# Performance work log

Hardware: AMD Instinct MI355X
Metric: run time of the kernel (lower is better)

The kernel has to match this reference:

```python
import jax, jax.numpy as jnp
import numpy as np

B, T, FB, C = 2, 256, 128, 128
H_T, H_F, BAND = 4, 4, 16
INNER = 4 * C


def setup_inputs() -> dict:
    key = jax.random.key(0)
    ks = jax.random.split(key, 8)
    g = lambda k, shp: jax.random.normal(k, shp, jnp.float32) * 0.02
    return {
        "x": jax.random.normal(ks[0], (B, T, FB, C), jnp.float32),
        # temporal pre-norm + MHA (in_proj [3C,C], out_proj [C,C])
        "ln_t_w": jnp.ones((C,), jnp.float32), "ln_t_b": jnp.zeros((C,), jnp.float32),
        "t_wi": g(ks[1], (3 * C, C)), "t_bi": jnp.zeros((3 * C,), jnp.float32),
        "t_wo": g(ks[2], (C, C)), "t_bo": jnp.zeros((C,), jnp.float32),
        # frequency pre-norm + MHA
        "ln_f_w": jnp.ones((C,), jnp.float32), "ln_f_b": jnp.zeros((C,), jnp.float32),
        "f_wi": g(ks[3], (3 * C, C)), "f_bi": jnp.zeros((3 * C,), jnp.float32),
        "f_wo": g(ks[4], (C, C)), "f_bo": jnp.zeros((C,), jnp.float32),
        # FFN pre-norm + two linears
        "ln_n_w": jnp.ones((C,), jnp.float32), "ln_n_b": jnp.zeros((C,), jnp.float32),
        "w1": g(ks[5], (INNER, C)), "b1": jnp.zeros((INNER,), jnp.float32),
        "w2": g(ks[6], (C, INNER)), "b2": jnp.zeros((C,), jnp.float32),
    }


def _ln(x, w, b, eps=1e-5):
    mu = x.mean(-1, keepdims=True)
    var = ((x - mu) ** 2).mean(-1, keepdims=True)
    return (x - mu) * jax.lax.rsqrt(var + eps) * w + b


def _mha(x, wi, bi, wo, bo, h, mask):
    """torch.nn.MultiheadAttention equivalent. x: [..., S, C], mask: additive [S, S]."""
    c = x.shape[-1]
    dh = c // h
    qkv = x @ wi.T + bi
    q, k, v = jnp.split(qkv, 3, axis=-1)
    split = lambda t: t.reshape(t.shape[:-1] + (h, dh)).swapaxes(-2, -3)  # [..., h, S, dh]
    q, k, v = split(q), split(k), split(v)
    scores = jnp.einsum('...hqd,...hkd->...hqk', q, k) * (1.0 / np.sqrt(dh)) + mask
    attn = jax.nn.softmax(scores, axis=-1)
    o = jnp.einsum('...hqk,...hkd->...hqd', attn, v)
    o = o.swapaxes(-2, -3).reshape(x.shape)
    return o @ wo.T + bo


def _causal_mask(n):
    i = jnp.arange(n)
    return jnp.where(i[:, None] >= i[None, :], 0.0, -jnp.inf).astype(jnp.float32)


def _band_mask(n, band):
    i = jnp.arange(n)
    return jnp.where(jnp.abs(i[:, None] - i[None, :]) <= band, 0.0, -jnp.inf).astype(jnp.float32)


def reference(x, ln_t_w, ln_t_b, t_wi, t_bi, t_wo, t_bo,
              ln_f_w, ln_f_b, f_wi, f_bi, f_wo, f_bo,
              ln_n_w, ln_n_b, w1, b1, w2, b2):
    cm = _causal_mask(x.shape[1])      # [T, T]
    bm = _band_mask(x.shape[2], BAND)  # [F, F]
    # temporal causal MHSA per frequency bin (pre-norm residual)
    xt = _ln(x, ln_t_w, ln_t_b).transpose(0, 2, 1, 3)  # [B, F, T, C]
    x = x + _mha(xt, t_wi, t_bi, t_wo, t_bo, H_T, cm).transpose(0, 2, 1, 3)
    # banded local MHSA over frequency per time step
    xf = _ln(x, ln_f_w, ln_f_b)  # [B, T, F, C]
    x = x + _mha(xf, f_wi, f_bi, f_wo, f_bo, H_F, bm)
    # FFN (Linear -> exact GELU -> Linear)
    xn = _ln(x, ln_n_w, ln_n_b)
    h = jax.nn.gelu(xn @ w1.T + b1, approximate=False)
    x = x + (h @ w2.T + b2)
    return x
```

## Files before the change

kernel.cpp:

```cpp
#include <hip/hip_runtime.h>
#include <math.h>

typedef __bf16 bf16;
typedef __bf16 bf16x8 __attribute__((ext_vector_type(8)));
typedef __bf16 bf16x4 __attribute__((ext_vector_type(4)));
typedef __bf16 bf16x2 __attribute__((ext_vector_type(2)));
typedef float f32x4 __attribute__((ext_vector_type(4)));
typedef float f32x2 __attribute__((ext_vector_type(2)));
typedef float f32x16 __attribute__((ext_vector_type(16)));
typedef unsigned int u32;
typedef unsigned int u32x4 __attribute__((ext_vector_type(4)));

#define AS1 __attribute__((address_space(1)))
#define AS3 __attribute__((address_space(3)))

static __device__ __forceinline__ f32x4 mfma16(bf16x8 a, bf16x8 b, f32x4 c) {
    return __builtin_amdgcn_mfma_f32_16x16x32_bf16(a, b, c, 0, 0, 0);
}
static __device__ __forceinline__ f32x16 mfma32(bf16x8 a, bf16x8 b, f32x16 c) {
    return __builtin_amdgcn_mfma_f32_32x32x16_bf16(a, b, c, 0, 0, 0);
}
static __device__ __forceinline__ u32 pk2(float a, float b) {
    bf16x2 v; v[0] = (bf16)a; v[1] = (bf16)b;
    return __builtin_bit_cast(u32, v);
}
static __device__ __forceinline__ float gelu_f(float x) {
    float u = 0.7978845608f * x * __builtin_fmaf(0.044715f, x * x, 1.0f);
    float e = __expf(2.0f * u);
    return x - x * __builtin_amdgcn_rcpf(e + 1.0f);
}

__global__ __launch_bounds__(256) void cvt_w6(
    const float* __restrict__ s0, const float* __restrict__ s1,
    const float* __restrict__ s2, const float* __restrict__ s3,
    const float* __restrict__ s4, const float* __restrict__ s5,
    bf16* __restrict__ dst)
{
    int i = (blockIdx.x * 256 + threadIdx.x) * 4;
    const float* src; int off;
    if      (i <  49152) { src = s0; off = 0; }
    else if (i <  65536) { src = s1; off = 49152; }
    else if (i < 114688) { src = s2; off = 65536; }
    else if (i < 131072) { src = s3; off = 114688; }
    else if (i < 196608) { src = s4; off = 131072; }
    else                 { src = s5; off = 196608; }
    f32x4 v = *(const f32x4*)&src[i - off];
    bf16x4 b;
    b[0] = (bf16)v[0]; b[1] = (bf16)v[1]; b[2] = (bf16)v[2]; b[3] = (bf16)v[3];
    *(bf16x4*)&dst[i] = b;
}

template<int OUT_BF16, int RES, int RESBF, int GELU_, int LNA, int RMAP, int KT, int NT>
__global__ __launch_bounds__(256) void gemm_rw(
    const bf16* __restrict__ A, const bf16* __restrict__ W,
    const float* __restrict__ bias, const void* __restrict__ res,
    void* __restrict__ outp,
    const float* __restrict__ xf, const float* __restrict__ lnaw,
    const float* __restrict__ lnab)
{
    constexpr int N = NT * 128;
    __shared__ __align__(16) bf16 Bs[128 * 64];
    const int tid  = threadIdx.x;
    const int lane = tid & 63;
    const int w    = tid >> 6;
    const int li = lane & 15, g = lane >> 4;
    const int m0 = blockIdx.x * 64;
    const int arow = m0 + w * 16 + li;
    int srow = arow;
    if constexpr (RMAP) {
        int b = arow >> 15, t = (arow >> 7) & 255, f = arow & 127;
        srow = (b << 15) + (f << 8) + t;
    }
    const bf16* ap = A + (size_t)srow * KT;

    bf16x8 afrag[4];
    if constexpr (LNA) {
        int b = arow >> 15, f = (arow >> 8) & 127, t = arow & 255;
        const float* xp = xf + (((size_t)b * 256 + t) * 128 + f) * 128;
        f32x4 cv[8];
        #pragma unroll
        for (int cc = 0; cc < 4; ++cc) {
            cv[2 * cc]     = *(const f32x4*)&xp[cc * 32 + g * 8];
            cv[2 * cc + 1] = *(const f32x4*)&xp[cc * 32 + g * 8 + 4];
        }
        float sm = 0.f, sq = 0.f;
        #pragma unroll
        for (int i = 0; i < 8; ++i)
            #pragma unroll
            for (int j = 0; j < 4; ++j) { float v = cv[i][j]; sm += v; sq += v * v; }
        sm += __shfl_xor(sm, 16); sm += __shfl_xor(sm, 32);
        sq += __shfl_xor(sq, 16); sq += __shfl_xor(sq, 32);
        float mu = sm * 0.0078125f;
        float rs = rsqrtf(sq * 0.0078125f - mu * mu + 1e-5f);
        #pragma unroll
        for (int cc = 0; cc < 4; ++cc) {
            f32x4 w0 = *(const f32x4*)&lnaw[cc * 32 + g * 8];
            f32x4 w1 = *(const f32x4*)&lnaw[cc * 32 + g * 8 + 4];
            f32x4 b0 = *(const f32x4*)&lnab[cc * 32 + g * 8];
            f32x4 b1 = *(const f32x4*)&lnab[cc * 32 + g * 8 + 4];
            #pragma unroll
            for (int j = 0; j < 4; ++j) {
                afrag[cc][j]     = (bf16)((cv[2 * cc][j]     - mu) * rs * w0[j] + b0[j]);
                afrag[cc][4 + j] = (bf16)((cv[2 * cc + 1][j] - mu) * rs * w1[j] + b1[j]);
            }
        }
    } else if constexpr (KT == 128) {
        #pragma unroll
        for (int cc = 0; cc < 4; ++cc)
            afrag[cc] = *(const bf16x8*)&ap[cc * 32 + g * 8];
    }

    #pragma unroll
    for (int t = 0; t < NT; ++t) {
        const int n0 = t * 128;
        f32x4 acc[8] = {};

        #pragma unroll
        for (int k0 = 0; k0 < KT; k0 += 64) {
            #pragma unroll
            for (int it = 0; it < 4; ++it) {
                int idx = it * 256 + tid;
                int brow = idx >> 3, bch = idx & 7;
                const bf16* gp = W + (size_t)(n0 + brow) * KT + k0 + ((bch ^ (brow & 7)) * 8);
                __builtin_amdgcn_global_load_lds((AS1 void*)gp, (AS3 void*)(Bs + idx * 8), 16, 0, 0);
            }
            bf16x8 av0, av1;
            if constexpr (KT != 128) {
                av0 = *(const bf16x8*)&ap[k0 + g * 8];
                av1 = *(const bf16x8*)&ap[k0 + 32 + g * 8];
            }
            __syncthreads();
            #pragma unroll
            for (int kk = 0; kk < 2; ++kk) {
                bf16x8 av;
                if constexpr (KT == 128) av = afrag[(k0 >> 5) + kk];
                else                     av = kk ? av1 : av0;
                #pragma unroll
                for (int j = 0; j < 8; ++j) {
                    int brow = j * 16 + li;
                    int bch = (kk * 4 + g) ^ (li & 7);
                    bf16x8 bv = *(const bf16x8*)&Bs[brow * 64 + bch * 8];
                    acc[j] = mfma16(av, bv, acc[j]);
                }
            }
            __syncthreads();
        }

        float bcol[8];
        #pragma unroll
        for (int j = 0; j < 8; ++j) bcol[j] = bias[n0 + j * 16 + li];

        const int row0 = m0 + w * 16 + g * 4;
        #pragma unroll
        for (int r = 0; r < 4; ++r) {
            int row = row0 + r;
            #pragma unroll
            for (int j = 0; j < 8; ++j) {
                size_t off = (size_t)row * N + n0 + j * 16 + li;
                float v = acc[j][r] + bcol[j];
                if constexpr (RES) {
                    if constexpr (RESBF) v += (float)((const bf16*)res)[off];
                    else                 v += ((const float*)res)[off];
                }
                if constexpr (GELU_) v = gelu_f(v);
                if constexpr (OUT_BF16) ((bf16*)outp)[off] = (bf16)v;
                else                    ((float*)outp)[off] = v;
            }
        }
    }
}

__global__ __launch_bounds__(256) void ffn_fused(
    const bf16* __restrict__ A, const bf16* __restrict__ W1,
    const float* __restrict__ b1, const bf16* __restrict__ W2,
    const float* __restrict__ b2, const bf16* __restrict__ res,
    float* __restrict__ outp)
{
    __shared__ __align__(16) bf16 Bs[2][128 * 64];
    __shared__ __align__(16) bf16 hbuf[64 * 136];
    const int tid  = threadIdx.x;
    const int lane = tid & 63;
    const int w    = tid >> 6;
    const int li = lane & 15, g = lane >> 4;
    const int m0 = blockIdx.x * 64;
    const int arow = m0 + w * 16 + li;
    const bf16* ap = A + (size_t)arow * 128;

    bf16x8 axn[4];
    #pragma unroll
    for (int cc = 0; cc < 4; ++cc)
        axn[cc] = *(const bf16x8*)&ap[cc * 32 + g * 8];

    auto stageW1 = [&](int b, int t, int k0) {
        #pragma unroll
        for (int it = 0; it < 4; ++it) {
            int idx = it * 256 + tid;
            int brow = idx >> 3, bch = idx & 7;
            const bf16* gp = W1 + (size_t)(t * 128 + brow) * 128 + k0 + ((bch ^ (brow & 7)) * 8);
            __builtin_amdgcn_global_load_lds((AS1 void*)gp, (AS3 void*)(Bs[b] + idx * 8), 16, 0, 0);
        }
    };
    auto stageW2 = [&](int b, int t, int k0) {
        #pragma unroll
        for (int it = 0; it < 4; ++it) {
            int idx = it * 256 + tid;
            int brow = idx >> 3, bch = idx & 7;
            const bf16* gp = W2 + (size_t)brow * 512 + t * 128 + k0 + ((bch ^ (brow & 7)) * 8);
            __builtin_amdgcn_global_load_lds((AS1 void*)gp, (AS3 void*)(Bs[b] + idx * 8), 16, 0, 0);
        }
    };
    auto compute16 = [&](int b, bf16x8 av0, bf16x8 av1, f32x4* acc) {
        #pragma unroll
        for (int kk = 0; kk < 2; ++kk) {
            bf16x8 av = kk ? av1 : av0;
            #pragma unroll
            for (int j = 0; j < 8; ++j) {
                int brow = j * 16 + li;
                int bch = (kk * 4 + g) ^ (li & 7);
                bf16x8 bv = *(const bf16x8*)&Bs[b][brow * 64 + bch * 8];
                acc[j] = mfma16(av, bv, acc[j]);
            }
        }
    };

    f32x4 oacc[8] = {};

    stageW1(0, 0, 0);
    stageW1(1, 0, 64);

    #pragma unroll
    for (int t = 0; t < 4; ++t) {
        f32x4 hacc[8] = {};

        asm volatile("s_waitcnt vmcnt(4)" ::: "memory");
        __builtin_amdgcn_s_barrier();
        __builtin_amdgcn_sched_barrier(0);
        compute16(0, axn[0], axn[1], hacc);
        __builtin_amdgcn_sched_barrier(0);
        __builtin_amdgcn_s_barrier();
        stageW2(0, t, 0);

        asm volatile("s_waitcnt vmcnt(4)" ::: "memory");
        __builtin_amdgcn_s_barrier();
        __builtin_amdgcn_sched_barrier(0);
        compute16(1, axn[2], axn[3], hacc);
        __builtin_amdgcn_sched_barrier(0);
        __builtin_amdgcn_s_barrier();
        stageW2(1, t, 64);

        float b1c[8];
        #pragma unroll
        for (int j = 0; j < 8; ++j) b1c[j] = b1[t * 128 + j * 16 + li];
        #pragma unroll
        for (int r = 0; r < 4; ++r) {
            int lrow = w * 16 + g * 4 + r;
            #pragma unroll
            for (int j = 0; j < 8; ++j)
                hbuf[lrow * 136 + j * 16 + li] = (bf16)gelu_f(hacc[j][r] + b1c[j]);
        }
        bf16x8 ah[4];
        #pragma unroll
        for (int cc = 0; cc < 4; ++cc)
            ah[cc] = *(const bf16x8*)&hbuf[(w * 16 + li) * 136 + cc * 32 + g * 8];

        asm volatile("s_waitcnt vmcnt(4)" ::: "memory");
        __builtin_amdgcn_s_barrier();
        __builtin_amdgcn_sched_barrier(0);
        compute16(0, ah[0], ah[1], oacc);
        __builtin_amdgcn_sched_barrier(0);
        __builtin_amdgcn_s_barrier();
        if (t < 3) stageW1(0, t + 1, 0);

        if (t < 3) asm volatile("s_waitcnt vmcnt(4)" ::: "memory");
        else       asm volatile("s_waitcnt vmcnt(0)" ::: "memory");
        __builtin_amdgcn_s_barrier();
        __builtin_amdgcn_sched_barrier(0);
        compute16(1, ah[2], ah[3], oacc);
        __builtin_amdgcn_sched_barrier(0);
        __builtin_amdgcn_s_barrier();
        if (t < 3) stageW1(1, t + 1, 64);
    }

    float b2c[8];
    #pragma unroll
    for (int j = 0; j < 8; ++j) b2c[j] = b2[j * 16 + li];
    const int row0 = m0 + w * 16 + g * 4;
    #pragma unroll
    for (int r = 0; r < 4; ++r) {
        int row = row0 + r;
        #pragma unroll
        for (int j = 0; j < 8; ++j) {
            size_t off = (size_t)row * 128 + j * 16 + li;
            outp[off] = oacc[j][r] + b2c[j] + (float)res[off];
        }
    }
}

template<int MODE, int RESBF>
__global__ __launch_bounds__(256) void attn_fused(
    const bf16* __restrict__ qkv, const bf16* __restrict__ Wo,
    const float* __restrict__ bo, const void* __restrict__ res,
    bf16* __restrict__ xc, bf16* __restrict__ xn,
    const float* __restrict__ lnw, const float* __restrict__ lnb)
{
    constexpr int S = (MODE == 0) ? 256 : 128;
    __shared__ __align__(16) char smem[2 * 20480 + 2048];
    float* red = (float*)(smem + 40960);
    const int tid = threadIdx.x;
    const int lane = tid & 63;
    const int w = tid >> 6;
    const int hi = lane >> 5;
    const int q31 = lane & 31;
    const int s = blockIdx.x;
    const int qb = blockIdx.y * 64;

    const size_t base = (size_t)s * S * 384;
    const bf16* qp = qkv + base + w * 32;

    const float sc = 0.17677669529663687f;
    bf16x8 qA0, qA1, qB0, qB1;
    {
        bf16x8 r0 = *(const bf16x8*)&qp[(size_t)(qb + q31) * 384 + hi * 8];
        bf16x8 r1 = *(const bf16x8*)&qp[(size_t)(qb + q31) * 384 + 16 + hi * 8];
        bf16x8 r2 = *(const bf16x8*)&qp[(size_t)(qb + 32 + q31) * 384 + hi * 8];
        bf16x8 r3 = *(const bf16x8*)&qp[(size_t)(qb + 32 + q31) * 384 + 16 + hi * 8];
        #pragma unroll
        for (int e = 0; e < 8; ++e) {
            qA0[e] = (bf16)((float)r0[e] * sc);
            qA1[e] = (bf16)((float)r1[e] * sc);
            qB0[e] = (bf16)((float)r2[e] * sc);
            qB1[e] = (bf16)((float)r3[e] * sc);
        }
    }

    f32x16 OA = {}, OB = {};
    float lA = 0.f, lB = 0.f;

    int klo, khi;
    if constexpr (MODE == 0) { klo = 0; khi = qb + 64; }
    else {
        klo = (qb > 16 ? (qb - 16) : 0) & ~31;
        khi = (qb + 80 < S) ? (qb + 80) : S;
    }

    const int seg = tid & 15, rw = tid >> 4;
    const char* qc = (const char*)qkv + base * 2;
    const int wdst = (seg >> 2) * 2560 + rw * 80 + (seg & 3) * 16;

    u32x4 rk0, rk1, rv0, rv1;
    auto gload = [&](int k0) {
        const char* r0 = qc + (size_t)(k0 + rw) * 768;
        const char* r1 = qc + (size_t)(k0 + rw + 16) * 768;
        rk0 = *(const u32x4*)(r0 + 256 + seg * 16);
        rk1 = *(const u32x4*)(r1 + 256 + seg * 16);
        rv0 = *(const u32x4*)(r0 + 512 + seg * 16);
        rv1 = *(const u32x4*)(r1 + 512 + seg * 16);
    };
    auto swrite = [&](char* buf) {
        *(u32x4*)(buf + wdst)                = rk0;
        *(u32x4*)(buf + wdst + 1280)         = rk1;
        *(u32x4*)(buf + 10240 + wdst)        = rv0;
        *(u32x4*)(buf + 10240 + wdst + 1280) = rv1;
    };

    gload(klo);
    swrite(smem);
    __syncthreads();
    int cur = 0;

    for (int k0 = klo; k0 < khi; k0 += 32) {
        bool notlast = (k0 + 32 < khi);
        if (notlast) gload(k0 + 32);

        char* buf = smem + cur * 20480;
        const char* kb = buf + w * 2560 + q31 * 80 + hi * 16;
        bf16x8 kf0 = *(const bf16x8*)(kb);
        bf16x8 kf1 = *(const bf16x8*)(kb + 32);
        const bf16* vb = (const bf16*)(buf + 10240) + w * 1280 + hi * 320 + q31;
        bf16x8 vf1, vf2;
        #pragma unroll
        for (int e = 0; e < 8; ++e) {
            vf1[e] = vb[e * 40];
            vf2[e] = vb[640 + e * 40];
        }

        auto step = [&](f32x16& O, float& l, bf16x8 q0, bf16x8 q1,
                        int qrow, bool doMask) {
            f32x16 st = {};
            st = mfma32(kf0, q0, st);
            st = mfma32(kf1, q1, st);
            if (doMask) {
                #pragma unroll
                for (int r = 0; r < 16; ++r) {
                    int krow = k0 + (r & 3) + 8 * (r >> 2) + 4 * hi;
                    bool ok;
                    if constexpr (MODE == 0) ok = (krow <= qrow);
                    else { int d = krow - qrow; ok = (d <= 16 && d >= -16); }
                    st[r] = ok ? st[r] : -3.0e38f;
                }
            }
            float ps = 0.f;
            #pragma unroll
            for (int r = 0; r < 16; ++r) {
                float p = __expf(st[r]);
                st[r] = p;
                ps += p;
            }
            ps += __shfl_xor(ps, 32);
            l += ps;

            u32 c01 = pk2(st[0], st[1]),   c23 = pk2(st[2], st[3]);
            u32 c45 = pk2(st[4], st[5]),   c67 = pk2(st[6], st[7]);
            u32 c89 = pk2(st[8], st[9]),   cAB = pk2(st[10], st[11]);
            u32 cCD = pk2(st[12], st[13]), cEF = pk2(st[14], st[15]);
            u32 x01 = __shfl_xor((int)c01, 32), x23 = __shfl_xor((int)c23, 32);
            u32 x45 = __shfl_xor((int)c45, 32), x67 = __shfl_xor((int)c67, 32);
            u32 x89 = __shfl_xor((int)c89, 32), xAB = __shfl_xor((int)cAB, 32);
            u32 xCD = __shfl_xor((int)cCD, 32), xEF = __shfl_xor((int)cEF, 32);
            u32x4 b1w = hi ? u32x4{x45, x67, c45, c67} : u32x4{c01, c23, x01, x23};
            u32x4 b2w = hi ? u32x4{xCD, xEF, cCD, cEF} : u32x4{c89, cAB, x89, xAB};
            bf16x8 B1 = __builtin_bit_cast(bf16x8, b1w);
            bf16x8 B2 = __builtin_bit_cast(bf16x8, b2w);

            O = mfma32(vf1, B1, O);
            O = mfma32(vf2, B2, O);
        };

        bool actA, actB, dgA, dgB;
        if constexpr (MODE == 0) {
            actA = (k0 <= qb); actB = true;
            dgA = (k0 == qb);  dgB = (k0 == qb + 32);
        } else {
            actA = (k0 >= qb - 47) && (k0 <= qb + 47);
            actB = (k0 >= qb - 15) && (k0 <= qb + 79);
            dgA = true; dgB = true;
        }
        if (actA) step(OA, lA, qA0, qA1, qb + q31, dgA);
        if (actB) step(OB, lB, qB0, qB1, qb + 32 + q31, dgB);

        if (notlast) swrite(smem + (cur ^ 1) * 20480);
        __syncthreads();
        cur ^= 1;
    }

    bf16* o_lds = (bf16*)smem;
    float invA = 1.f / lA, invB = 1.f / lB;
    #pragma unroll
    for (int mb = 0; mb < 4; ++mb) {
        bf16x4 ovA, ovB;
        #pragma unroll
        for (int j = 0; j < 4; ++j) {
            ovA[j] = (bf16)(OA[mb * 4 + j] * invA);
            ovB[j] = (bf16)(OB[mb * 4 + j] * invB);
        }
        *(bf16x4*)&o_lds[q31 * 136 + w * 32 + mb * 8 + hi * 4] = ovA;
        *(bf16x4*)&o_lds[(32 + q31) * 136 + w * 32 + mb * 8 + hi * 4] = ovB;
    }
    __syncthreads();

    const int li = lane & 15, g = lane >> 4;
    bf16x8 af[4][4];
    #pragma unroll
    for (int mi = 0; mi < 4; ++mi)
        #pragma unroll
        for (int kk = 0; kk < 4; ++kk)
            af[mi][kk] = *(const bf16x8*)&o_lds[(mi * 16 + li) * 136 + kk * 32 + g * 8];

    f32x4 acc[4][2] = {};
    #pragma unroll
    for (int ni = 0; ni < 2; ++ni) {
        #pragma unroll
        for (int kk = 0; kk < 4; ++kk) {
            bf16x8 bv = *(const bf16x8*)&Wo[(size_t)(w * 32 + ni * 16 + li) * 128 + kk * 32 + g * 8];
            #pragma unroll
            for (int mi = 0; mi < 4; ++mi)
                acc[mi][ni] = mfma16(af[mi][kk], bv, acc[mi][ni]);
        }
    }

    float vals[4][2][4];
    #pragma unroll
    for (int mi = 0; mi < 4; ++mi) {
        #pragma unroll
        for (int r = 0; r < 4; ++r) {
            int lrl = mi * 16 + g * 4 + r;
            int grow = qb + lrl;
            size_t rrow;
            if constexpr (MODE == 0) {
                int b = s >> 7, f = s & 127;
                rrow = ((size_t)(b * 256 + grow)) * 128 + f;
            } else {
                int b = s >> 8, t = s & 255;
                rrow = (size_t)b * 32768 + (size_t)grow * 256 + t;
            }
            #pragma unroll
            for (int ni = 0; ni < 2; ++ni) {
                int col = w * 32 + ni * 16 + li;
                float v = acc[mi][ni][r] + bo[col];
                if constexpr (RESBF) v += (float)((const bf16*)res)[rrow * 128 + col];
                else                 v += ((const float*)res)[rrow * 128 + col];
                vals[mi][ni][r] = v;
            }
        }
    }
    #pragma unroll
    for (int mi = 0; mi < 4; ++mi) {
        #pragma unroll
        for (int r = 0; r < 4; ++r) {
            float sm = vals[mi][0][r] + vals[mi][1][r];
            float sq = vals[mi][0][r] * vals[mi][0][r] + vals[mi][1][r] * vals[mi][1][r];
            #pragma unroll
            for (int off = 1; off < 16; off <<= 1) {
                sm += __shfl_xor(sm, off);
                sq += __shfl_xor(sq, off);
            }
            if (li == 0) {
                red[(mi * 16 + g * 4 + r) * 8 + w * 2 + 0] = sm;
                red[(mi * 16 + g * 4 + r) * 8 + w * 2 + 1] = sq;
            }
        }
    }
    __syncthreads();
    #pragma unroll
    for (int mi = 0; mi < 4; ++mi) {
        #pragma unroll
        for (int r = 0; r < 4; ++r) {
            int mrow = mi * 16 + g * 4 + r;
            f32x4 p0 = *(const f32x4*)&red[mrow * 8 + 0];
            f32x4 p1 = *(const f32x4*)&red[mrow * 8 + 4];
            float smt = p0[0] + p0[2] + p1[0] + p1[2];
            float sqt = p0[1] + p0[3] + p1[1] + p1[3];
            float mu = smt * 0.0078125f;
            float rs = rsqrtf(sqt * 0.0078125f - mu * mu + 1e-5f);
            size_t woff = ((size_t)s * S + qb + mrow) * 128;
            #pragma unroll
            for (int ni = 0; ni < 2; ++ni) {
                int col = w * 32 + ni * 16 + li;
                float v = vals[mi][ni][r];
                xc[woff + col] = (bf16)v;
                xn[woff + col] = (bf16)((v - mu) * rs * lnw[col] + lnb[col]);
            }
        }
    }
}

extern "C" void kernel_launch(void* const* d_in, const int* in_sizes, int n_in,
                              void* d_out, int out_size, void* d_ws, size_t ws_size,
                              hipStream_t stream) {
    const float* x      = (const float*)d_in[0];
    const float* ln_t_w = (const float*)d_in[1];
    const float* ln_t_b = (const float*)d_in[2];
    const float* t_wi   = (const float*)d_in[3];
    const float* t_bi   = (const float*)d_in[4];
    const float* t_wo   = (const float*)d_in[5];
    const float* t_bo   = (const float*)d_in[6];
    const float* ln_f_w = (const float*)d_in[7];
    const float* ln_f_b = (const float*)d_in[8];
    const float* f_wi   = (const float*)d_in[9];
    const float* f_bi   = (const float*)d_in[10];
    const float* f_wo   = (const float*)d_in[11];
    const float* f_bo   = (const float*)d_in[12];
    const float* ln_n_w = (const float*)d_in[13];
    const float* ln_n_b = (const float*)d_in[14];
    const float* w1     = (const float*)d_in[15];
    const float* b1     = (const float*)d_in[16];
    const float* w2     = (const float*)d_in[17];
    const float* b2     = (const float*)d_in[18];

    char* ws = (char*)d_ws;
    bf16* wbf  = (bf16*)ws;
    bf16* xn   = (bf16*)(ws + 524288);
    bf16* qkvh = (bf16*)(ws + 524288 + 16777216);
    bf16* xcA  = (bf16*)(ws + 524288 + 16777216 + 67108864 + 16777216);
    bf16* xcB  = (bf16*)(ws + 524288 + 16777216 + 67108864 + 2 * 16777216);
    float* out = (float*)d_out;

    const bf16* twi_b = wbf + 0;
    const bf16* two_b = wbf + 49152;
    const bf16* fwi_b = wbf + 65536;
    const bf16* fwo_b = wbf + 114688;
    const bf16* w1_b  = wbf + 131072;
    const bf16* w2_b  = wbf + 196608;

    cvt_w6<<<256, 256, 0, stream>>>(t_wi, t_wo, f_wi, f_wo, w1, w2, wbf);

    gemm_rw<1, 0, 0, 0, 1, 0, 128, 3><<<1024, 256, 0, stream>>>(
        nullptr, twi_b, t_bi, nullptr, qkvh, x, ln_t_w, ln_t_b);
    attn_fused<0, 0><<<dim3(256, 4), 256, 0, stream>>>(
        qkvh, two_b, t_bo, x, xcA, xn, ln_f_w, ln_f_b);

    gemm_rw<1, 0, 0, 0, 0, 1, 128, 3><<<1024, 256, 0, stream>>>(
        xn, fwi_b, f_bi, nullptr, qkvh, nullptr, nullptr, nullptr);
    attn_fused<1, 1><<<dim3(512, 2), 256, 0, stream>>>(
        qkvh, fwo_b, f_bo, xcA, xcB, xn, ln_n_w, ln_n_b);

    ffn_fused<<<1024, 256, 0, stream>>>(xn, w1_b, b1, w2_b, b2, xcB, out);

    (void)in_sizes; (void)n_in; (void)out_size; (void)ws_size;
}
```

Measured before the change: 148.1 us.

## Double-buffer weight tiles in gemm_rw to overlap loads with MFMA

Restructures the gemm_rw weight loop into a flat stage sequence over N-tiles and K-halves. Each stage's tile is prefetched into one of two LDS buffers while the other is consumed, using vmcnt waits and explicit barriers. All N-tile accumulators are kept live and the epilogue runs afterwards. This hides global-to-LDS latency at the cost of doubled LDS (32KB) and NT*32 accumulator registers, which may reduce occupancy for larger NT such as the QKV projection.

```diff
diff --git a/kernel.cpp b/kernel.cpp
--- a/kernel.cpp
+++ b/kernel.cpp
@@ -59,7 +59,8 @@
     const float* __restrict__ lnab)
 {
     constexpr int N = NT * 128;
-    __shared__ __align__(16) bf16 Bs[128 * 64];
+    static_assert(KT == 128, "pipelined gemm_rw assumes KT==128");
+    __shared__ __align__(16) bf16 Bs[2][128 * 64];
     const int tid  = threadIdx.x;
     const int lane = tid & 63;
     const int w    = tid >> 6;
@@ -104,60 +105,64 @@
                 afrag[cc][4 + j] = (bf16)((cv[2 * cc + 1][j] - mu) * rs * w1[j] + b1[j]);
             }
         }
-    } else if constexpr (KT == 128) {
+    } else {
         #pragma unroll
         for (int cc = 0; cc < 4; ++cc)
             afrag[cc] = *(const bf16x8*)&ap[cc * 32 + g * 8];
     }
 
+    auto stage = [&](int s) {
+        int t = s >> 1, k0 = (s & 1) * 64;
+        #pragma unroll
+        for (int it = 0; it < 4; ++it) {
+            int idx = it * 256 + tid;
+            int brow = idx >> 3, bch = idx & 7;
+            const bf16* gp = W + (size_t)(t * 128 + brow) * KT + k0 + ((bch ^ (brow & 7)) * 8);
+            __builtin_amdgcn_global_load_lds((AS1 void*)gp, (AS3 void*)(Bs[s & 1] + idx * 8), 16, 0, 0);
+        }
+    };
+
+    f32x4 acc[NT][8] = {};
+
+    stage(0);
+    stage(1);
+    #pragma unroll
+    for (int s = 0; s < 2 * NT; ++s) {
+        if (s < 2 * NT - 1) asm volatile("s_waitcnt vmcnt(4)" ::: "memory");
+        else                asm volatile("s_waitcnt vmcnt(0)" ::: "memory");
+        __builtin_amdgcn_s_barrier();
+        __builtin_amdgcn_sched_barrier(0);
+        const int t = s >> 1;
+        #pragma unroll
+        for (int kk = 0; kk < 2; ++kk) {
+            bf16x8 av = afrag[2 * (s & 1) + kk];
+            #pragma unroll
+            for (int j = 0; j < 8; ++j) {
+                int brow = j * 16 + li;
+                int bch = (kk * 4 + g) ^ (li & 7);
+                bf16x8 bv = *(const bf16x8*)&Bs[s & 1][brow * 64 + bch * 8];
+                acc[t][j] = mfma16(av, bv, acc[t][j]);
+            }
+        }
+        __builtin_amdgcn_sched_barrier(0);
+        __builtin_amdgcn_s_barrier();
+        if (s + 2 < 2 * NT) stage(s + 2);
+    }
+
+    const int row0 = m0 + w * 16 + g * 4;
     #pragma unroll
     for (int t = 0; t < NT; ++t) {
         const int n0 = t * 128;
-        f32x4 acc[8] = {};
-
-        #pragma unroll
-        for (int k0 = 0; k0 < KT; k0 += 64) {
-            #pragma unroll
-            for (int it = 0; it < 4; ++it) {
-                int idx = it * 256 + tid;
-                int brow = idx >> 3, bch = idx & 7;
-                const bf16* gp = W + (size_t)(n0 + brow) * KT + k0 + ((bch ^ (brow & 7)) * 8);
-                __builtin_amdgcn_global_load_lds((AS1 void*)gp, (AS3 void*)(Bs + idx * 8), 16, 0, 0);
-            }
-            bf16x8 av0, av1;
-            if constexpr (KT != 128) {
-                av0 = *(const bf16x8*)&ap[k0 + g * 8];
-                av1 = *(const bf16x8*)&ap[k0 + 32 + g * 8];
-            }
-            __syncthreads();
-            #pragma unroll
-            for (int kk = 0; kk < 2; ++kk) {
-                bf16x8 av;
-                if constexpr (KT == 128) av = afrag[(k0 >> 5) + kk];
-                else                     av = kk ? av1 : av0;
-                #pragma unroll
-                for (int j = 0; j < 8; ++j) {
-                    int brow = j * 16 + li;
-                    int bch = (kk * 4 + g) ^ (li & 7);
-                    bf16x8 bv = *(const bf16x8*)&Bs[brow * 64 + bch * 8];
-                    acc[j] = mfma16(av, bv, acc[j]);
-                }
-            }
-            __syncthreads();
-        }
-
         float bcol[8];
         #pragma unroll
         for (int j = 0; j < 8; ++j) bcol[j] = bias[n0 + j * 16 + li];
-
-        const int row0 = m0 + w * 16 + g * 4;
         #pragma unroll
         for (int r = 0; r < 4; ++r) {
             int row = row0 + r;
             #pragma unroll
             for (int j = 0; j < 8; ++j) {
                 size_t off = (size_t)row * N + n0 + j * 16 + li;
-                float v = acc[j][r] + bcol[j];
+                float v = acc[t][j][r] + bcol[j];
                 if constexpr (RES) {
                     if constexpr (RESBF) v += (float)((const bf16*)res)[off];
                     else                 v += ((const float*)res)[off];
```

Result: slower. 158.1 us (+6.8%).
